# Performance work log

Hardware: AMD Instinct MI355X
Metric: run time of the kernel (lower is better)

The kernel has to match this reference:

```python
import jax, jax.numpy as jnp
import numpy as np

D_MODEL, D_STATE, D_CONV, D_INNER, DT_RANK = 1024, 16, 4, 2048, 64
B_SZ, L = 2, 2048


def setup_inputs() -> dict:
    key = jax.random.key(0)
    ks = jax.random.split(key, 12)
    s = 0.02
    return {
        "x": jax.random.normal(ks[0], (B_SZ, L, D_MODEL), jnp.float32),
        "in_proj_w": jax.random.normal(ks[1], (2 * D_INNER, D_MODEL), jnp.float32) * s,
        "conv_w": jax.random.normal(ks[2], (D_INNER, 1, D_CONV), jnp.float32) * 0.1,
        "conv_b": jnp.zeros((D_INNER,), jnp.float32),
        "A_log": jax.random.normal(ks[3], (D_INNER, D_STATE), jnp.float32) * 0.1,
        "D": jnp.ones((D_INNER,), jnp.float32),
        "dt_proj_w": jax.random.uniform(ks[4], (D_INNER, DT_RANK), jnp.float32, -DT_RANK ** -0.5, DT_RANK ** -0.5),
        "dt_proj_b": jax.random.uniform(ks[5], (D_INNER,), jnp.float32, -5.0, -3.0),
        "x_proj_w": jax.random.normal(ks[6], (DT_RANK, D_INNER), jnp.float32) * s,
        "B_proj_w": jax.random.normal(ks[7], (D_STATE, D_INNER), jnp.float32) * s,
        "C_proj_w": jax.random.normal(ks[8], (D_STATE, D_INNER), jnp.float32) * s,
        "out_proj_w": jax.random.normal(ks[9], (D_MODEL, D_INNER), jnp.float32) * s,
    }


def _causal_depthwise_conv(x, w, b):
    # x: (b, L, d_inner); w: (d_inner, 1, d_conv); left-pad (d_conv-1) zeros = conv1d(padding=d_conv-1)[..., :L]
    xt = jnp.transpose(x, (0, 2, 1))  # (b, d_inner, L)
    xt = jnp.pad(xt, ((0, 0), (0, 0), (w.shape[-1] - 1, 0)))
    out = jax.lax.conv_general_dilated(
        xt, w, window_strides=(1,), padding="VALID",
        dimension_numbers=("NCW", "OIW", "NCW"), feature_group_count=w.shape[0])
    return jnp.transpose(out + b[None, :, None], (0, 2, 1))  # (b, L, d_inner)


def _selective_scan(x, dt, A, B, C):
    # x, dt: (b, L, d_inner); A: (d_inner, d_state); B, C: (b, L, d_state)
    b, seq_len, d_inner = x.shape
    h0 = jnp.zeros((b, d_inner, A.shape[1]), x.dtype)

    def step(h, inp):
        xt, dtt, Bt, Ct = inp  # (b,di) (b,di) (b,ds) (b,ds)
        dte = dtt[..., None]                         # (b, di, 1)
        h = h + dte * (A[None] * h) + dte * (Bt[:, None, :] * xt[..., None])
        yt = jnp.einsum("bns,bs->bn", h, Ct)
        return h, yt

    inputs = (jnp.swapaxes(x, 0, 1), jnp.swapaxes(dt, 0, 1),
              jnp.swapaxes(B, 0, 1), jnp.swapaxes(C, 0, 1))
    _, y = jax.lax.scan(step, h0, inputs)
    return jnp.swapaxes(y, 0, 1)  # (b, L, d_inner)


def _forward(x, in_proj_w, conv_w, conv_b, A_log, D, dt_proj_w, dt_proj_b,
             x_proj_w, B_proj_w, C_proj_w, out_proj_w):
    xz = x @ in_proj_w.T                         # (b, L, 2*d_inner)
    x_in, z = jnp.split(xz, 2, axis=-1)
    x_conv = jax.nn.silu(_causal_depthwise_conv(x_in, conv_w, conv_b))
    dt = jax.nn.softplus((x_conv @ x_proj_w.T) @ dt_proj_w.T + dt_proj_b)
    B = x_conv @ B_proj_w.T                      # (b, L, d_state)
    C = x_conv @ C_proj_w.T
    A = -jnp.exp(A_log)
    y = _selective_scan(x_conv, dt, A, B, C)
    y = y + D[None, None, :] * x_conv
    y = y * jax.nn.silu(z)
    return y @ out_proj_w.T                      # (b, L, d_model)


def reference(x, in_proj_w, conv_w, conv_b, A_log, D, dt_proj_w, dt_proj_b,
              x_proj_w, B_proj_w, C_proj_w, out_proj_w):
    return _forward(x, in_proj_w, conv_w, conv_b, A_log, D, dt_proj_w, dt_proj_b,
                    x_proj_w, B_proj_w, C_proj_w, out_proj_w)
```

## Files before the change

### kernel.cpp

```cpp
#include <hip/hip_runtime.h>
#include <hip/hip_bf16.h>
#include <math.h>

using bf16 = __hip_bfloat16;
typedef short bf16x8 __attribute__((ext_vector_type(8)));
typedef float f32x4  __attribute__((ext_vector_type(4)));

#define DMODEL 1024
#define DSTATE 16
#define DCONV  4
#define DINNER 2048
#define DTRANK 64
#define BSZ    2
#define LSEQ   2048
#define MROWS  (BSZ*LSEQ)

#define NCHUNK 32
#define CHUNK  (LSEQ / NCHUNK)
#define DS_TOT (DINNER * DSTATE)
#define NBCX   96

__device__ __forceinline__ float cvt(float v) { return v; }
__device__ __forceinline__ float cvt(bf16 v)  { return __bfloat162float(v); }

template<typename T> __device__ __forceinline__ T sto(float v);
template<> __device__ __forceinline__ float sto<float>(float v) { return v; }
template<> __device__ __forceinline__ bf16  sto<bf16>(float v)  { return __float2bfloat16(v); }

__device__ __forceinline__ void gll16(const bf16* g, short* l)
{
    __builtin_amdgcn_global_load_lds(
        (const __attribute__((address_space(1))) unsigned int*)(const void*)g,
        (__attribute__((address_space(3))) unsigned int*)(void*)l,
        16, 0, 0);
}

__global__ __launch_bounds__(256)
void cvt_all(const float* __restrict__ a, const float* __restrict__ b,
             const float* __restrict__ c, const float* __restrict__ d,
             const float* __restrict__ xp, const float* __restrict__ Bp,
             const float* __restrict__ Cp,
             bf16* __restrict__ oa, bf16* __restrict__ ob, bf16* __restrict__ oc,
             bf16* __restrict__ od, bf16* __restrict__ obcx,
             int na, int nb, int nc, int nd, int nbcx)
{
    const int idx = (blockIdx.x * 256 + threadIdx.x) * 4;
    const float* src; bf16* dst; int off;
    if (idx < na)                      { src = a; dst = oa; off = idx; }
    else if (idx < na + nb)            { src = b; dst = ob; off = idx - na; }
    else if (idx < na + nb + nc)       { src = c; dst = oc; off = idx - na - nb; }
    else if (idx < na + nb + nc + nd)  { src = d; dst = od; off = idx - na - nb - nc; }
    else if (idx < na+nb+nc+nd+nbcx) {
        off = idx - na - nb - nc - nd;
        const int r = off >> 11, k = off & 2047;
        src = (r < 64) ? (xp + (size_t)r * 2048 + k)
            : (r < 80) ? (Bp + (size_t)(r - 64) * 2048 + k)
                       : (Cp + (size_t)(r - 80) * 2048 + k);
        src -= off;
        dst = obcx;
    } else return;
    const float4 v = *(const float4*)(src + off);
    dst[off + 0] = sto<bf16>(v.x); dst[off + 1] = sto<bf16>(v.y);
    dst[off + 2] = sto<bf16>(v.z); dst[off + 3] = sto<bf16>(v.w);
}

template<typename TO, int SPLITK, int EPI>
__global__ __launch_bounds__(256)
void gemm_mfma(const bf16* __restrict__ A, const bf16* __restrict__ W,
               TO* __restrict__ out, TO* __restrict__ out2,
               const float* __restrict__ bias,
               int M, int N, int K, int split, int kchunk)
{
    __shared__ __align__(16) short smem[16384];
    short* As = smem;
    short* Bs = smem + 8192;

    const int tid  = threadIdx.x;
    const int lane = tid & 63;
    const int wv   = tid >> 6;
    const int wm = (wv & 1) * 64;
    const int wn = (wv >> 1) * 64;
    const int m0 = blockIdx.y * 128;
    const int n0 = blockIdx.x * 128;

    const int p0 = wv * 64 + lane;
    const int p1 = p0 + 256;
    const int r0 = p0 >> 2, c0 = (p0 & 3) ^ ((r0 >> 1) & 3);
    const int r1 = p1 >> 2, c1 = (p1 & 3) ^ ((r1 >> 1) & 3);

    const bf16* srcA0 = A + (size_t)(m0 + r0) * K + c0 * 8;
    const bf16* srcA1 = A + (size_t)(m0 + r1) * K + c1 * 8;
    int nr0 = n0 + r0; if (nr0 >= N) nr0 = N - 1;
    int nr1 = n0 + r1; if (nr1 >= N) nr1 = N - 1;
    const bf16* srcB0 = W + (size_t)nr0 * K + c0 * 8;
    const bf16* srcB1 = W + (size_t)nr1 * K + c1 * 8;

    const int C4 = lane >> 4;
    const int fr = lane & 15;
    int aOff[4], bOff[4];
    #pragma unroll
    for (int i = 0; i < 4; ++i) {
        const int R = wm + i * 16 + fr;
        aOff[i] = R * 32 + ((C4 ^ ((R >> 1) & 3)) << 3);
    }
    #pragma unroll
    for (int j = 0; j < 4; ++j) {
        const int R = wn + j * 16 + fr;
        bOff[j] = R * 32 + ((C4 ^ ((R >> 1) & 3)) << 3);
    }

    f32x4 acc[4][4] = {};

    const int kb  = blockIdx.z * kchunk;
    const int nit = kchunk / 32;

    gll16(srcA0 + kb, &As[wv * 512]);
    gll16(srcA1 + kb, &As[(wv + 4) * 512]);
    gll16(srcB0 + kb, &Bs[wv * 512]);
    gll16(srcB1 + kb, &Bs[(wv + 4) * 512]);

    for (int it = 0; it < nit; ++it) {
        __syncthreads();
        const int p = it & 1;
        if (it + 1 < nit) {
            const int q  = p ^ 1;
            const int k1 = kb + (it + 1) * 32;
            gll16(srcA0 + k1, &As[q * 4096 + wv * 512]);
            gll16(srcA1 + k1, &As[q * 4096 + (wv + 4) * 512]);
            gll16(srcB0 + k1, &Bs[q * 4096 + wv * 512]);
            gll16(srcB1 + k1, &Bs[q * 4096 + (wv + 4) * 512]);
        }
        bf16x8 af[4], bfr[4];
        #pragma unroll
        for (int i = 0; i < 4; ++i) af[i]  = *(const bf16x8*)&As[p * 4096 + aOff[i]];
        #pragma unroll
        for (int j = 0; j < 4; ++j) bfr[j] = *(const bf16x8*)&Bs[p * 4096 + bOff[j]];
        #pragma unroll
        for (int i = 0; i < 4; ++i)
            #pragma unroll
            for (int j = 0; j < 4; ++j)
                acc[i][j] = __builtin_amdgcn_mfma_f32_16x16x32_bf16(af[i], bfr[j], acc[i][j], 0, 0, 0);
    }

    __syncthreads();

    const int rb = (lane >> 4) * 4;

    if constexpr (sizeof(TO) == 2) {
        bf16* cs = (bf16*)smem;
        #pragma unroll
        for (int i = 0; i < 4; ++i)
            #pragma unroll
            for (int j = 0; j < 4; ++j)
                #pragma unroll
                for (int r = 0; r < 4; ++r) {
                    const int m = wm + i * 16 + rb + r;
                    const int n = wn + j * 16 + fr;
                    float v = acc[i][j][r];
                    if (EPI == 1) {
                        v += bias[n0 + n];
                        v = (v > 20.f) ? v : log1pf(expf(v));
                    }
                    const int key = (m >> 2) & 3;
                    cs[m * 128 + (n ^ ((key & 1) << 4) ^ ((key >> 1) << 5))] = sto<bf16>(v);
                }
        __syncthreads();
        TO* ob; int nc0; int ostr;
        if (split > 0) {
            if (n0 < split) { ob = out;  nc0 = n0;         }
            else            { ob = out2; nc0 = n0 - split; }
            ostr = split;
        } else { ob = out; nc0 = n0; ostr = N; }
        #pragma unroll
        for (int g8 = 0; g8 < 8; ++g8) {
            const int G = tid + 256 * g8;
            const int mrow = G >> 4;
            const int cg = G & 15;
            const int key = (mrow >> 2) & 3;
            const int nst = (cg * 8) ^ ((key & 1) << 4) ^ ((key >> 1) << 5);
            if (n0 + nst < N) {
                const uint4 val = *(const uint4*)&cs[mrow * 128 + cg * 8];
                *(uint4*)&ob[(size_t)(m0 + mrow) * ostr + nc0 + nst] = val;
            }
        }
    } else {
        float* fs = (float*)smem;
        float* obase = SPLITK ? ((float*)out + (size_t)blockIdx.z * M * N) : (float*)out;
        #pragma unroll
        for (int ph = 0; ph < 2; ++ph) {
            __syncthreads();
            if ((wn >> 6) == ph) {
                #pragma unroll
                for (int i = 0; i < 4; ++i)
                    #pragma unroll
                    for (int j = 0; j < 4; ++j)
                        #pragma unroll
                        for (int r = 0; r < 4; ++r) {
                            const int m = wm + i * 16 + rb + r;
                            const int qq = j * 16 + fr;
                            fs[m * 64 + (qq ^ (((m >> 2) & 1) << 4))] = acc[i][j][r];
                        }
            }
            __syncthreads();
            #pragma unroll
            for (int g8 = 0; g8 < 8; ++g8) {
                const int G = tid + 256 * g8;
                const int mrow = G >> 4;
                const int cg = G & 15;
                const int qst = (cg * 4) ^ (((mrow >> 2) & 1) << 4);
                const int n_g = 64 * ph + qst;
                if (n0 + n_g < N) {
                    const float4 val = *(const float4*)&fs[mrow * 64 + cg * 4];
                    *(float4*)&obase[(size_t)(m0 + mrow) * N + n0 + n_g] = val;
                }
            }
        }
    }
}

__global__ __launch_bounds__(256)
void reduce_bcx(const float* __restrict__ P8, bf16* __restrict__ xr,
                float* __restrict__ BC)
{
    const int u = blockIdx.x * 256 + threadIdx.x;
    const int m = u / NBCX;
    const int n = u - m * NBCX;
    float s = 0.f;
    #pragma unroll
    for (int k = 0; k < 8; ++k) s += P8[(size_t)k * MROWS * NBCX + u];
    if (n < 64) xr[(size_t)m * 64 + n] = sto<bf16>(s);
    else        BC[(size_t)m * 32 + (n - 64)] = s;
}

__global__ __launch_bounds__(256)
void conv_silu(const bf16* __restrict__ x_in, const float* __restrict__ cw,
               const float* __restrict__ cb, bf16* __restrict__ x_conv)
{
    const size_t i8 = (size_t)(blockIdx.x * 256 + threadIdx.x) * 8;
    const int d = (int)(i8 & (DINNER - 1));
    const int t = (int)((i8 >> 11) & (LSEQ - 1));
    uint4 v[4];
    const uint4 z4 = make_uint4(0, 0, 0, 0);
    v[3] = *(const uint4*)(x_in + i8);
    v[2] = (t >= 1) ? *(const uint4*)(x_in + i8 - 1 * DINNER) : z4;
    v[1] = (t >= 2) ? *(const uint4*)(x_in + i8 - 2 * DINNER) : z4;
    v[0] = (t >= 3) ? *(const uint4*)(x_in + i8 - 3 * DINNER) : z4;
    const bf16* e0 = (const bf16*)&v[0];
    const bf16* e1 = (const bf16*)&v[1];
    const bf16* e2 = (const bf16*)&v[2];
    const bf16* e3 = (const bf16*)&v[3];
    bf16 ob[8];
    #pragma unroll
    for (int e = 0; e < 8; ++e) {
        const float4 w = *(const float4*)(cw + (size_t)(d + e) * 4);
        float a = cb[d + e];
        a = fmaf(w.x, cvt(e0[e]), a);
        a = fmaf(w.y, cvt(e1[e]), a);
        a = fmaf(w.z, cvt(e2[e]), a);
        a = fmaf(w.w, cvt(e3[e]), a);
        const float sig = 1.f / (1.f + __expf(-a));
        ob[e] = sto<bf16>(a * sig);
    }
    *(uint4*)(x_conv + i8) = *(const uint4*)ob;
}

__global__ __launch_bounds__(64)
void scan_phase_a(const bf16* __restrict__ x_conv, const bf16* __restrict__ dt,
                  const float* __restrict__ BC, const float* __restrict__ A_log,
                  float* __restrict__ hend, float* __restrict__ Pprod)
{
    const int lane = threadIdx.x;
    const int c = blockIdx.x;
    const int d = blockIdx.y * 64 + lane;
    const int b = blockIdx.z;

    float Af[DSTATE];
    #pragma unroll
    for (int s = 0; s < DSTATE; ++s) Af[s] = -__expf(A_log[d * DSTATE + s]);

    float h[DSTATE], P[DSTATE];
    #pragma unroll
    for (int s = 0; s < DSTATE; ++s) { h[s] = 0.f; P[s] = 1.f; }

    const size_t base = ((size_t)b * LSEQ + (size_t)c * CHUNK) * DINNER + d;
    const bf16* xp  = x_conv + base;
    const bf16* dtp = dt + base;
    const float* Bp = BC + ((size_t)b * LSEQ + (size_t)c * CHUNK) * 32;

    for (int t0 = 0; t0 < CHUNK; t0 += 4) {
        float xg[4], dtg[4];
        #pragma unroll
        for (int j = 0; j < 4; ++j) {
            xg[j]  = cvt(xp [(size_t)(t0 + j) * DINNER]);
            dtg[j] = cvt(dtp[(size_t)(t0 + j) * DINNER]);
        }
        #pragma unroll
        for (int j = 0; j < 4; ++j) {
            float Bv[DSTATE];
            const float* Br = Bp + (size_t)(t0 + j) * 32;
            *(float4*)(&Bv[0])  = *(const float4*)(Br + 0);
            *(float4*)(&Bv[4])  = *(const float4*)(Br + 4);
            *(float4*)(&Bv[8])  = *(const float4*)(Br + 8);
            *(float4*)(&Bv[12]) = *(const float4*)(Br + 12);
            const float dtv = dtg[j];
            const float dtx = dtv * xg[j];
            #pragma unroll
            for (int s = 0; s < DSTATE; ++s) {
                const float a = fmaf(dtv, Af[s], 1.0f);
                h[s] = fmaf(h[s], a, dtx * Bv[s]);
                P[s] *= a;
            }
        }
    }

    const size_t oidx = (((size_t)b * NCHUNK + c) * DINNER + d) * DSTATE;
    #pragma unroll
    for (int s = 0; s < DSTATE; ++s) {
        hend [oidx + s] = h[s];
        Pprod[oidx + s] = P[s];
    }
}

__global__ __launch_bounds__(256)
void scan_combine(float* __restrict__ hend, const float* __restrict__ Pprod)
{
    const int u = blockIdx.x * 256 + threadIdx.x;
    const int b = blockIdx.y;
    float h = 0.f;
    for (int c = 0; c < NCHUNK; ++c) {
        const size_t idx = ((size_t)b * NCHUNK + c) * DS_TOT + u;
        const float he = hend[idx];
        const float p  = Pprod[idx];
        hend[idx] = h;
        h = fmaf(p, h, he);
    }
}

__global__ __launch_bounds__(64)
void scan_phase_c(const bf16* __restrict__ x_conv, const bf16* __restrict__ dt,
                  const float* __restrict__ BC,
                  const float* __restrict__ A_log, const float* __restrict__ Dw,
                  const float* __restrict__ hin, bf16* __restrict__ zy)
{
    const int lane = threadIdx.x;
    const int c = blockIdx.x;
    const int d = blockIdx.y * 64 + lane;
    const int b = blockIdx.z;

    float Af[DSTATE];
    #pragma unroll
    for (int s = 0; s < DSTATE; ++s) Af[s] = -__expf(A_log[d * DSTATE + s]);
    const float Dv = Dw[d];

    float h[DSTATE];
    const size_t hidx = (((size_t)b * NCHUNK + c) * DINNER + d) * DSTATE;
    #pragma unroll
    for (int s = 0; s < DSTATE; ++s) h[s] = hin[hidx + s];

    const size_t base = ((size_t)b * LSEQ + (size_t)c * CHUNK) * DINNER + d;
    const bf16* xp  = x_conv + base;
    const bf16* dtp = dt + base;
    bf16*       zp  = zy + base;
    const float* Bp = BC + ((size_t)b * LSEQ + (size_t)c * CHUNK) * 32;
    const float* Cp = Bp + 16;

    for (int t0 = 0; t0 < CHUNK; t0 += 4) {
        float xg[4], dtg[4], zg[4];
        #pragma unroll
        for (int j = 0; j < 4; ++j) {
            xg[j]  = cvt(xp [(size_t)(t0 + j) * DINNER]);
            dtg[j] = cvt(dtp[(size_t)(t0 + j) * DINNER]);
            zg[j]  = cvt(zp [(size_t)(t0 + j) * DINNER]);
        }
        #pragma unroll
        for (int j = 0; j < 4; ++j) {
            float Bv[DSTATE], Cv[DSTATE];
            const float* Br = Bp + (size_t)(t0 + j) * 32;
            const float* Cr = Cp + (size_t)(t0 + j) * 32;
            *(float4*)(&Bv[0])  = *(const float4*)(Br + 0);
            *(float4*)(&Bv[4])  = *(const float4*)(Br + 4);
            *(float4*)(&Bv[8])  = *(const float4*)(Br + 8);
            *(float4*)(&Bv[12]) = *(const float4*)(Br + 12);
            *(float4*)(&Cv[0])  = *(const float4*)(Cr + 0);
            *(float4*)(&Cv[4])  = *(const float4*)(Cr + 4);
            *(float4*)(&Cv[8])  = *(const float4*)(Cr + 8);
            *(float4*)(&Cv[12]) = *(const float4*)(Cr + 12);
            const float dtv = dtg[j];
            const float dtx = dtv * xg[j];
            float y = 0.f;
            #pragma unroll
            for (int s = 0; s < DSTATE; ++s) {
                const float a = fmaf(dtv, Af[s], 1.0f);
                h[s] = fmaf(h[s], a, dtx * Bv[s]);
                y = fmaf(h[s], Cv[s], y);
            }
            const float zv = zg[j];
            const float sig = 1.f / (1.f + __expf(-zv));
            zp[(size_t)(t0 + j) * DINNER] = sto<bf16>(fmaf(Dv, xg[j], y) * (zv * sig));
        }
    }
}

extern "C" void kernel_launch(void* const* d_in, const int* in_sizes, int n_in,
                              void* d_out, int out_size, void* d_ws, size_t ws_size,
                              hipStream_t stream)
{
    const float* x          = (const float*)d_in[0];
    const float* in_proj_w  = (const float*)d_in[1];
    const float* conv_w     = (const float*)d_in[2];
    const float* conv_b     = (const float*)d_in[3];
    const float* A_log      = (const float*)d_in[4];
    const float* Dw         = (const float*)d_in[5];
    const float* dt_proj_w  = (const float*)d_in[6];
    const float* dt_proj_b  = (const float*)d_in[7];
    const float* x_proj_w   = (const float*)d_in[8];
    const float* B_proj_w   = (const float*)d_in[9];
    const float* C_proj_w   = (const float*)d_in[10];
    const float* out_proj_w = (const float*)d_in[11];
    float* out = (float*)d_out;

    const size_t MD = (size_t)MROWS * DINNER;
    bf16* buf0 = (bf16*)d_ws;
    bf16* buf1 = buf0 + MD;
    bf16* buf2 = buf1 + MD;
    bf16* xbf  = buf2 + MD;
    bf16* wbf1 = xbf  + (size_t)MROWS * DMODEL;
    bf16* wbf2 = wbf1 + (size_t)2 * DINNER * DMODEL;
    bf16* wbc  = wbf2 + (size_t)DMODEL * DINNER;
    bf16* wdt  = wbc  + (size_t)NBCX * DINNER;
    float* hend = (float*)(wdt + (size_t)DINNER * DTRANK);
    float* Pp   = hend + (size_t)BSZ * NCHUNK * DS_TOT;
    bf16*  xr_bf = xbf;
    float* BCbuf = (float*)(xbf + (size_t)MROWS * DTRANK);
    float* P8 = (float*)buf0;

    dim3 blk(256);
    const int na = MROWS * DMODEL;
    const int nb = 2 * DINNER * DMODEL;
    const int nc = DMODEL * DINNER;
    const int nd = DINNER * DTRANK;
    const int nbcx = NBCX * DINNER;

    cvt_all<<<(na + nb + nc + nd + nbcx) / 1024, blk, 0, stream>>>(
        x, in_proj_w, out_proj_w, dt_proj_w, x_proj_w, B_proj_w, C_proj_w,
        xbf, wbf1, wbf2, wdt, wbc, na, nb, nc, nd, nbcx);

    gemm_mfma<bf16, 0, 0><<<dim3(2 * DINNER / 128, MROWS / 128, 1), blk, 0, stream>>>(
        xbf, wbf1, buf0, buf1, nullptr, MROWS, 2 * DINNER, DMODEL, DINNER, DMODEL);

    conv_silu<<<(MROWS * DINNER) / (256 * 8), blk, 0, stream>>>(buf0, conv_w, conv_b, buf2);

    gemm_mfma<float, 1, 0><<<dim3(1, MROWS / 128, 8), blk, 0, stream>>>(
        buf2, wbc, P8, (float*)nullptr, nullptr, MROWS, NBCX, DINNER, 0, DINNER / 8);

    reduce_bcx<<<(MROWS * NBCX) / 256, blk, 0, stream>>>(P8, xr_bf, BCbuf);

    gemm_mfma<bf16, 0, 1><<<dim3(DINNER / 128, MROWS / 128, 1), blk, 0, stream>>>(
        xr_bf, wdt, buf0, (bf16*)nullptr, dt_proj_b, MROWS, DINNER, DTRANK, 0, DTRANK);

    scan_phase_a<<<dim3(NCHUNK, DINNER / 64, BSZ), dim3(64), 0, stream>>>(
        buf2, buf0, BCbuf, A_log, hend, Pp);
    scan_combine<<<dim3(DS_TOT / 256, BSZ), dim3(256), 0, stream>>>(hend, Pp);
    scan_phase_c<<<dim3(NCHUNK, DINNER / 64, BSZ), dim3(64), 0, stream>>>(
        buf2, buf0, BCbuf, A_log, Dw, hend, buf1);

    gemm_mfma<float, 0, 0><<<dim3(DMODEL / 128, MROWS / 128, 1), blk, 0, stream>>>(
        buf1, wbf2, out, (float*)nullptr, nullptr, MROWS, DMODEL, DINNER, 0, DINNER);
}
```

Before: 321.0 us.

## Replace in_proj GEMM with 256x256-tile, 8-wave pipelined MFMA kernel

Adds a new gemm256 kernel for the input projection (4096x4096x1024). It uses 256x256 tiles with 512 threads, direct global-to-LDS loads into a swizzled double-buffered 128KB LDS layout, and fine-grained interleaving of LDS reads, prefetch and MFMA phases with barriers and s_setprio. It also remaps workgroups across XCDs and stages the output through LDS for coalesced 16-byte stores. The goal is higher MFMA utilisation and data reuse than the previous 128x128 kernel, at the cost of heavy LDS use, occupancy limits and code that depends on exact wait counts.

```diff
diff --git a/kernel.cpp b/kernel.cpp
--- a/kernel.cpp
+++ b/kernel.cpp
@@ -62,6 +62,141 @@
     const float4 v = *(const float4*)(src + off);
     dst[off + 0] = sto<bf16>(v.x); dst[off + 1] = sto<bf16>(v.y);
     dst[off + 2] = sto<bf16>(v.z); dst[off + 3] = sto<bf16>(v.w);
+}
+
+#define BAR   __builtin_amdgcn_s_barrier()
+#define LGK0  asm volatile("s_waitcnt lgkmcnt(0)" ::: "memory")
+#define VM4   asm volatile("s_waitcnt vmcnt(4)" ::: "memory")
+#define VM0   asm volatile("s_waitcnt vmcnt(0)" ::: "memory")
+#define PRIO1 __builtin_amdgcn_s_setprio(1)
+#define PRIO0 __builtin_amdgcn_s_setprio(0)
+
+#define STAGE(PTR, SOFF, REGSH, T, H) \
+  { const bf16* s_ = (PTR) + (SOFF) + (size_t)(H)*128*K + (size_t)(T)*64; \
+    short* d_ = lds + (REGSH) + (H)*8192 + tid*8; \
+    gll16(s_, d_); gll16(s_ + rstep, d_ + 4096); }
+
+#define RD_A(BASE, MH) \
+  { _Pragma("unroll") \
+    for (int ii = 0; ii < 4; ++ii) { \
+      const int fb_ = (BASE) + ((MH)*4 + ii) * 2048; \
+      a_[ii][0] = *(const bf16x8*)(ldsB + (fb_ + kc0)); \
+      a_[ii][1] = *(const bf16x8*)(ldsB + (fb_ + kc1)); } }
+
+#define RD_B(BASE, NH, B_) \
+  { _Pragma("unroll") \
+    for (int jj = 0; jj < 2; ++jj) { \
+      const int fb_ = (BASE) + ((NH)*2 + jj) * 2048; \
+      B_[jj][0] = *(const bf16x8*)(ldsB + (fb_ + kc0)); \
+      B_[jj][1] = *(const bf16x8*)(ldsB + (fb_ + kc1)); } }
+
+#define MM(MH, NH, B_) \
+  { _Pragma("unroll") \
+    for (int ii = 0; ii < 4; ++ii) { \
+      _Pragma("unroll") \
+      for (int jj = 0; jj < 2; ++jj) { \
+        f32x4& c_ = acc[(MH)*4 + ii][(NH)*2 + jj]; \
+        c_ = __builtin_amdgcn_mfma_f32_16x16x32_bf16(a_[ii][0], B_[jj][0], c_, 0, 0, 0); \
+        c_ = __builtin_amdgcn_mfma_f32_16x16x32_bf16(a_[ii][1], B_[jj][1], c_, 0, 0, 0); } } }
+
+__global__ __launch_bounds__(512, 2)
+void gemm256(const bf16* __restrict__ A, const bf16* __restrict__ W,
+             bf16* __restrict__ out0, bf16* __restrict__ out1,
+             int N, int K, int split)
+{
+    __shared__ __align__(16) short lds[65536];
+
+    const int tid  = threadIdx.x;
+    const int lane = tid & 63;
+    const int wv   = tid >> 6;
+    const int wm_i = wv >> 2;
+    const int wn_i = wv & 3;
+    const int fr   = lane & 15;
+    const int C4   = lane >> 4;
+
+    int wg = blockIdx.x;
+    { const int nwg = gridDim.x;
+      const int q = nwg >> 3, r = nwg & 7, x = wg & 7, o = wg >> 3;
+      wg = (x < r ? x * (q + 1) : r * (q + 1) + (x - r) * q) + o; }
+    const int nbx = N >> 8;
+    const int bx = wg % nbx, by = wg / nbx;
+    const int m0 = by * 256, n0 = bx * 256;
+
+    const int lr  = tid >> 3;
+    const int cbh = ((((tid & 7) << 4) ^ (((tid >> 3) & 7) << 4)) >> 1);
+    const size_t aso   = (size_t)(m0 + lr) * K + cbh;
+    const size_t bso   = (size_t)(n0 + lr) * K + cbh;
+    const size_t rstep = (size_t)64 * K;
+
+    const char* const ldsB = (const char*)lds;
+    const int xk  = (fr & 7) << 4;
+    const int kc0 = (C4 * 16) ^ xk;
+    const int kc1 = (64 + C4 * 16) ^ xk;
+    const int aRB0 = 0     + wm_i * 16384 + fr * 128;
+    const int aRB1 = 32768 + wm_i * 16384 + fr * 128;
+    const int bRB0 = 65536 + (wn_i >> 1) * 16384 + (wn_i & 1) * 8192 + fr * 128;
+    const int bRB1 = 98304 + (wn_i >> 1) * 16384 + (wn_i & 1) * 8192 + fr * 128;
+
+    f32x4  acc[8][4] = {};
+    bf16x8 a_[4][2], b0_[2][2], b1_[2][2];
+
+    STAGE(A, aso, 0,     0, 0); STAGE(A, aso, 0,     0, 1);
+    STAGE(W, bso, 32768, 0, 0); STAGE(W, bso, 32768, 0, 1);
+    STAGE(W, bso, 49152, 1, 0); STAGE(W, bso, 49152, 1, 1);
+    VM0; BAR;
+
+    const int NIT = K >> 7;
+    for (int it = 0; it < NIT; ++it) {
+        const int tA1 = 2 * it + 1;
+        const int tN  = 2 * it + 2;
+        const bool pf = (it + 1 < NIT);
+        RD_A(aRB0, 0); RD_B(bRB0, 0, b0_);
+        STAGE(A, aso, 16384, tA1, 0);
+        BAR; LGK0; PRIO1; MM(0, 0, b0_); PRIO0; BAR;
+        RD_B(bRB0, 1, b1_);
+        STAGE(A, aso, 16384, tA1, 1);
+        BAR; LGK0; PRIO1; MM(0, 1, b1_); PRIO0; BAR;
+        RD_A(aRB0, 1);
+        if (pf) STAGE(W, bso, 32768, tN, 0);
+        BAR; LGK0; PRIO1; MM(1, 0, b0_); PRIO0; BAR;
+        if (pf) { STAGE(W, bso, 32768, tN, 1); VM4; } else { VM0; }
+        BAR; LGK0; PRIO1; MM(1, 1, b1_); PRIO0; BAR;
+        RD_A(aRB1, 0); RD_B(bRB1, 0, b0_);
+        if (pf) STAGE(A, aso, 0, tN, 0);
+        BAR; LGK0; PRIO1; MM(0, 0, b0_); PRIO0; BAR;
+        RD_B(bRB1, 1, b1_);
+        if (pf) STAGE(A, aso, 0, tN, 1);
+        BAR; LGK0; PRIO1; MM(0, 1, b1_); PRIO0; BAR;
+        RD_A(aRB1, 1);
+        if (pf) STAGE(W, bso, 49152, 2 * it + 3, 0);
+        BAR; LGK0; PRIO1; MM(1, 0, b0_); PRIO0; BAR;
+        if (pf) { STAGE(W, bso, 49152, 2 * it + 3, 1); VM4; }
+        BAR; LGK0; PRIO1; MM(1, 1, b1_); PRIO0; BAR;
+    }
+
+    bf16* cs = (bf16*)lds;
+    #pragma unroll
+    for (int i = 0; i < 8; ++i)
+        #pragma unroll
+        for (int j = 0; j < 4; ++j)
+            #pragma unroll
+            for (int r = 0; r < 4; ++r) {
+                const int m = wm_i * 128 + i * 16 + C4 * 4 + r;
+                const int n = wn_i * 64  + j * 16 + fr;
+                cs[m * 256 + (n ^ ((m & 7) << 3))] = sto<bf16>(acc[i][j][r]);
+            }
+    __syncthreads();
+    bf16* dst; int colb;
+    if (n0 < split) { dst = out0; colb = n0; }
+    else            { dst = out1; colb = n0 - split; }
+    #pragma unroll
+    for (int g = 0; g < 16; ++g) {
+        const int G = tid + 512 * g;
+        const int m = G >> 5;
+        const int c = G & 31;
+        const uint4 v = *(const uint4*)&cs[m * 256 + ((c * 8) ^ ((m & 7) << 3))];
+        *(uint4*)&dst[(size_t)(m0 + m) * split + colb + c * 8] = v;
+    }
 }
 
 template<typename TO, int SPLITK, int EPI>
@@ -445,8 +580,8 @@
         x, in_proj_w, out_proj_w, dt_proj_w, x_proj_w, B_proj_w, C_proj_w,
         xbf, wbf1, wbf2, wdt, wbc, na, nb, nc, nd, nbcx);
 
-    gemm_mfma<bf16, 0, 0><<<dim3(2 * DINNER / 128, MROWS / 128, 1), blk, 0, stream>>>(
-        xbf, wbf1, buf0, buf1, nullptr, MROWS, 2 * DINNER, DMODEL, DINNER, DMODEL);
+    gemm256<<<dim3((MROWS / 256) * (2 * DINNER / 256)), dim3(512), 0, stream>>>(
+        xbf, wbf1, buf0, buf1, 2 * DINNER, DMODEL, DINNER);
 
     conv_silu<<<(MROWS * DINNER) / (256 * 8), blk, 0, stream>>>(buf0, conv_w, conv_b, buf2);
 
```

Result: faster. 312.9 us (-2.5%).
